# Kernel optimization log

Hardware: AMD Instinct MI355X
Metric: run time of the kernel (lower is better)

Reference implementation:

```python
import jax, jax.numpy as jnp
import numpy as np

EMBED_DIM = 1024
NUM_HEADS = 16
D_K = EMBED_DIM // NUM_HEADS
SEQ = 4096
BATCH = 1


def setup_inputs() -> dict:
    key = jax.random.key(0)
    ks = jax.random.split(key, 9)
    s = 1.0 / np.sqrt(EMBED_DIM)
    return {
        "x": jax.random.normal(ks[0], (BATCH, SEQ, EMBED_DIM), dtype=jnp.float32),
        "Wq": jax.random.normal(ks[1], (EMBED_DIM, EMBED_DIM), dtype=jnp.float32) * s,
        "bq": jax.random.normal(ks[2], (EMBED_DIM,), dtype=jnp.float32) * 0.02,
        "Wk": jax.random.normal(ks[3], (EMBED_DIM, EMBED_DIM), dtype=jnp.float32) * s,
        "bk": jax.random.normal(ks[4], (EMBED_DIM,), dtype=jnp.float32) * 0.02,
        "Wv": jax.random.normal(ks[5], (EMBED_DIM, EMBED_DIM), dtype=jnp.float32) * s,
        "bv": jax.random.normal(ks[6], (EMBED_DIM,), dtype=jnp.float32) * 0.02,
        "Wo": jax.random.normal(ks[7], (EMBED_DIM, EMBED_DIM), dtype=jnp.float32) * s,
        "bo": jax.random.normal(ks[8], (EMBED_DIM,), dtype=jnp.float32) * 0.02,
    }


def reference(x, Wq, bq, Wk, bk, Wv, bv, Wo, bo):
    B, S, E = x.shape
    H, Dk = NUM_HEADS, D_K

    def split_heads(t):  # [B,S,E] -> [B,H,S,Dk]
        return t.reshape(B, S, H, Dk).transpose(0, 2, 1, 3)

    Q = split_heads(x @ Wq.T + bq)
    K = split_heads(x @ Wk.T + bk)
    V = split_heads(x @ Wv.T + bv)

    scores = jnp.einsum("bhqd,bhkd->bhqk", Q, K) / jnp.sqrt(jnp.float32(Dk))
    causal = jnp.tril(jnp.ones((S, S), dtype=bool))
    scores = jnp.where(causal, scores, -jnp.inf)
    attn = jax.nn.softmax(scores, axis=-1)
    out = jnp.einsum("bhqk,bhkd->bhqd", attn, V)  # [B,H,S,Dk]
    out = out.transpose(0, 2, 1, 3).reshape(B, S, E)
    return out @ Wo.T + bo
```

## Files before the change

kernel.cpp:

```cpp
#include <hip/hip_runtime.h>
#include <hip/hip_bf16.h>
#include <math.h>

#define SEQ 4096
#define EMB 1024
#define NH  16
#define DK  64

typedef __attribute__((ext_vector_type(8))) unsigned short us8;
typedef __attribute__((ext_vector_type(8))) short         s8;
typedef __attribute__((ext_vector_type(4))) unsigned short us4;
typedef __attribute__((ext_vector_type(4))) float          f4;

static __device__ __forceinline__ unsigned short f2bf(float f) {
    union { float f; unsigned u; } v; v.f = f;
    unsigned r = v.u + 0x7FFF + ((v.u >> 16) & 1);
    return (unsigned short)(r >> 16);
}

__device__ __forceinline__ void gl2lds16(const void* g, void* l) {
    __builtin_amdgcn_global_load_lds((const __attribute__((address_space(1))) void*)g,
                                     (__attribute__((address_space(3))) void*)l, 16, 0, 0);
}

__device__ __forceinline__ int pkbf(float a, float b) {
    return (int)__builtin_amdgcn_perm(__float_as_uint(a), __float_as_uint(b), 0x07060302u);
}

__global__ void cvt_all(const float* __restrict__ x,
                        const float* __restrict__ w0, const float* __restrict__ w1,
                        const float* __restrict__ w2, const float* __restrict__ w3,
                        unsigned short* __restrict__ xo,
                        unsigned short* __restrict__ o0, unsigned short* __restrict__ o1,
                        unsigned short* __restrict__ o2, unsigned short* __restrict__ o3) {
    const int idx = blockIdx.x * 256 + threadIdx.x;
    const float* in;
    unsigned short* out;
    int off;
    if (idx < (1 << 20)) { in = x; out = xo; off = idx; }
    else {
        const int t = idx - (1 << 20);
        const int w = t >> 18;
        off = t & ((1 << 18) - 1);
        in  = w == 0 ? w0 : (w == 1 ? w1 : (w == 2 ? w2 : w3));
        out = w == 0 ? o0 : (w == 1 ? o1 : (w == 2 ? o2 : o3));
    }
    const float4 v = ((const float4*)in)[off];
    us4 o;
    o[0] = f2bf(v.x); o[1] = f2bf(v.y); o[2] = f2bf(v.z); o[3] = f2bf(v.w);
    ((us4*)out)[off] = o;
}

__global__ __launch_bounds__(256) void transpose_kernel(
    const unsigned short* __restrict__ in, unsigned short* __restrict__ out) {
    __shared__ unsigned short t[64][72];
    const int tid = threadIdx.x;
    const int row = tid >> 2, c = (tid & 3) * 16;
    const int gr = blockIdx.x * 64, gc = blockIdx.y * 64;
    const unsigned short* src = in + (size_t)(gr + row) * EMB + gc + c;
    *(us8*)&t[row][c]     = *(const us8*)src;
    *(us8*)&t[row][c + 8] = *(const us8*)(src + 8);
    __syncthreads();
    us8 o0, o1;
#pragma unroll
    for (int j = 0; j < 8; ++j) { o0[j] = t[c + j][row]; o1[j] = t[c + 8 + j][row]; }
    const int a_   = c >> 4;
    const int base = (a_ >> 1) * 32 + (a_ & 1) * 4;
    us4 g0, g1, g2, g3;
#pragma unroll
    for (int i = 0; i < 4; ++i) { g0[i] = o0[i]; g1[i] = o0[4 + i]; g2[i] = o1[i]; g3[i] = o1[4 + i]; }
    unsigned short* dst = out + (size_t)(gc + row) * SEQ + gr + base;
    *(us4*)dst        = g0;
    *(us4*)(dst + 8)  = g1;
    *(us4*)(dst + 16) = g2;
    *(us4*)(dst + 24) = g3;
}

__global__ __launch_bounds__(256) void qkv_gemm(
    const unsigned short* __restrict__ X,
    const unsigned short* __restrict__ Wq, const unsigned short* __restrict__ Wk,
    const unsigned short* __restrict__ Wv,
    const float* __restrict__ bq, const float* __restrict__ bk, const float* __restrict__ bv,
    unsigned short* __restrict__ Qo, unsigned short* __restrict__ Ko, unsigned short* __restrict__ Vo)
{
    __shared__ unsigned short As[128 * 64];
    __shared__ unsigned short Bs[128 * 64];

    const int region = blockIdx.y >> 3;
    const unsigned short* W   = region == 0 ? Wq : (region == 1 ? Wk : Wv);
    const float*         bias = region == 0 ? bq : (region == 1 ? bk : bv);
    unsigned short*      out  = region == 0 ? Qo : (region == 1 ? Ko : Vo);
    const float scale = region == 0 ? 0.18033688011112042f : 1.0f;

    const int tid  = threadIdx.x;
    const int wave = tid >> 6;
    const int lane = tid & 63;
    const int quad = lane >> 4;
    const int l16  = lane & 15;
    const int wm   = (wave >> 1) * 64;
    const int wn   = (wave & 1) * 64;
    const int bm   = blockIdx.x * 128;
    const int bn   = (blockIdx.y & 7) * 128;

    f4 acc[4][4];
#pragma unroll
    for (int a = 0; a < 4; ++a)
#pragma unroll
        for (int b = 0; b < 4; ++b) acc[a][b] = (f4){0, 0, 0, 0};

    const int rsub = lane >> 3;
    const int gc   = ((lane & 7) ^ rsub) * 8;
    const int swz  = l16 & 7;

    for (int k0 = 0; k0 < EMB; k0 += 64) {
        __syncthreads();
#pragma unroll
        for (int i = 0; i < 4; ++i) {
            const int cb = i * 4 + wave;
            const int r  = cb * 8 + rsub;
            gl2lds16(X + (size_t)(bm + r) * EMB + k0 + gc, &As[cb * 512]);
            gl2lds16(W + (size_t)(bn + r) * EMB + k0 + gc, &Bs[cb * 512]);
        }
        __syncthreads();
#pragma unroll
        for (int kc = 0; kc < 2; ++kc) {
            s8 af[4], bf[4];
#pragma unroll
            for (int t = 0; t < 4; ++t) {
                const int seg = (kc * 4 + quad) ^ swz;
                af[t] = *(const s8*)&As[(wm + t * 16 + l16) * 64 + seg * 8];
                bf[t] = *(const s8*)&Bs[(wn + t * 16 + l16) * 64 + seg * 8];
            }
#pragma unroll
            for (int tm = 0; tm < 4; ++tm)
#pragma unroll
                for (int tn = 0; tn < 4; ++tn)
                    acc[tm][tn] = __builtin_amdgcn_mfma_f32_16x16x32_bf16(af[tm], bf[tn], acc[tm][tn], 0, 0, 0);
        }
    }

#pragma unroll
    for (int tn = 0; tn < 4; ++tn) {
        const int n = bn + wn + tn * 16 + l16;
        const float bv2 = bias[n];
#pragma unroll
        for (int tm = 0; tm < 4; ++tm)
#pragma unroll
            for (int rr = 0; rr < 4; ++rr) {
                const int m = bm + wm + tm * 16 + quad * 4 + rr;
                out[(size_t)m * EMB + n] = f2bf((acc[tm][tn][rr] + bv2) * scale);
            }
    }
}

__global__ __launch_bounds__(256) void gemm_op(
    const unsigned short* __restrict__ A, const unsigned short* __restrict__ B,
    const float* __restrict__ bias, float* __restrict__ C)
{
    __shared__ unsigned short As[128 * 64];
    __shared__ unsigned short Bs[64 * 64];

    const int tid  = threadIdx.x;
    const int wave = tid >> 6;
    const int lane = tid & 63;
    const int quad = lane >> 4;
    const int l16  = lane & 15;
    const int wm   = (wave >> 1) * 64;
    const int wn   = (wave & 1) * 32;
    const int bm   = blockIdx.x * 128;
    const int bn   = blockIdx.y * 64;

    f4 acc[4][2];
#pragma unroll
    for (int a = 0; a < 4; ++a) { acc[a][0] = (f4){0,0,0,0}; acc[a][1] = (f4){0,0,0,0}; }

    const int rsub = lane >> 3;
    const int gc   = ((lane & 7) ^ rsub) * 8;
    const int swz  = l16 & 7;

    for (int k0 = 0; k0 < EMB; k0 += 64) {
        __syncthreads();
#pragma unroll
        for (int i = 0; i < 6; ++i) {
            const int cb = i * 4 + wave;
            if (cb < 16) {
                gl2lds16(A + (size_t)(bm + cb * 8 + rsub) * EMB + k0 + gc, &As[cb * 512]);
            } else {
                const int c2 = cb - 16;
                gl2lds16(B + (size_t)(bn + c2 * 8 + rsub) * EMB + k0 + gc, &Bs[c2 * 512]);
            }
        }
        __syncthreads();
#pragma unroll
        for (int kc = 0; kc < 2; ++kc) {
            const int seg = (kc * 4 + quad) ^ swz;
            s8 af[4], bf[2];
#pragma unroll
            for (int t = 0; t < 4; ++t)
                af[t] = *(const s8*)&As[(wm + t * 16 + l16) * 64 + seg * 8];
#pragma unroll
            for (int t = 0; t < 2; ++t)
                bf[t] = *(const s8*)&Bs[(wn + t * 16 + l16) * 64 + seg * 8];
#pragma unroll
            for (int tm = 0; tm < 4; ++tm)
#pragma unroll
                for (int tn = 0; tn < 2; ++tn)
                    acc[tm][tn] = __builtin_amdgcn_mfma_f32_16x16x32_bf16(af[tm], bf[tn], acc[tm][tn], 0, 0, 0);
        }
    }

#pragma unroll
    for (int tn = 0; tn < 2; ++tn) {
        const int n = bn + wn + tn * 16 + l16;
        const float bv2 = bias[n];
#pragma unroll
        for (int tm = 0; tm < 4; ++tm)
#pragma unroll
            for (int rr = 0; rr < 4; ++rr) {
                const int m = bm + wm + tm * 16 + quad * 4 + rr;
                C[(size_t)m * EMB + n] = acc[tm][tn][rr] + bv2;
            }
    }
}

__global__ __launch_bounds__(512) void attn_kernel(
    const unsigned short* __restrict__ Qg, const unsigned short* __restrict__ Kg,
    const unsigned short* __restrict__ Vtg, unsigned short* __restrict__ Og)
{
    __shared__ unsigned short Ks[2][128][72];
    __shared__ unsigned short Vs[2][128][72];

    const int tid  = threadIdx.x;
    const int wave = tid >> 6;
    const int lane = tid & 63;
    const int quad = lane >> 4;
    const int l16  = lane & 15;
    const int h    = blockIdx.x;
    const int y    = blockIdx.y;
    const int u    = (y < 16) ? y : 47 - y;
    const int jmax = 63 - u;
    const int jmine = (wave < 4) ? jmax : u;
    const int tileMine = (wave < 4) ? (63 - u) : u;
    const int colbase = h * DK;
    const int wrow0 = tileMine * 64 + (wave & 3) * 16;
    const int q_own = wrow0 + l16;

    s8 qf[2];
    {
        const unsigned short* q = Qg + (size_t)q_own * EMB + colbase + quad * 8;
        qf[0] = *(const s8*)(q);
        qf[1] = *(const s8*)(q + 32);
    }

    const int row = tid >> 3;
    const int c0  = (tid & 7) * 8;
    const unsigned short* kptr = Kg  + (size_t)row * EMB + colbase + c0;
    const unsigned short* vptr = Vtg + (size_t)(colbase + row) * SEQ + c0;

    const int imax = jmax >> 1;

    {
        us8 a = *(const us8*)kptr;
        us8 b = *(const us8*)(kptr + (size_t)64 * EMB);
        us8 c = *(const us8*)vptr;
        us8 d = *(const us8*)(vptr + 64);
        *(us8*)&Ks[0][row][c0]      = a;
        *(us8*)&Ks[0][64 + row][c0] = b;
        *(us8*)&Vs[0][row][c0]      = c;
        *(us8*)&Vs[0][64 + row][c0] = d;
    }
    us8 kre = *(const us8*)(kptr + (size_t)2 * 64 * EMB);
    us8 kro = *(const us8*)(kptr + (size_t)3 * 64 * EMB);
    us8 vre = *(const us8*)(vptr + 2 * 64);
    us8 vro = *(const us8*)(vptr + 3 * 64);

    float l_i = 0.0f;
    f4 o[4];
#pragma unroll
    for (int t = 0; t < 4; ++t) o[t] = (f4){0, 0, 0, 0};

    for (int i = 0; i <= imax; ++i) {
        __syncthreads();
        const int cur = i & 1;
        if (i < imax) {
            const int nxt = cur ^ 1;
            *(us8*)&Ks[nxt][row][c0]      = kre;
            *(us8*)&Ks[nxt][64 + row][c0] = kro;
            *(us8*)&Vs[nxt][row][c0]      = vre;
            *(us8*)&Vs[nxt][64 + row][c0] = vro;
            if (i + 1 < imax) {
                const int je = 2 * (i + 2);
                kre = *(const us8*)(kptr + (size_t)je * 64 * EMB);
                vre = *(const us8*)(vptr + je * 64);
                const int jo = je + 1;
                if (jo <= jmax) {
                    kro = *(const us8*)(kptr + (size_t)jo * 64 * EMB);
                    vro = *(const us8*)(vptr + jo * 64);
                }
            }
        }

#pragma unroll
        for (int sub = 0; sub < 2; ++sub) {
            const int j = 2 * i + sub;
            if (j <= jmine) {
                const int rb = sub * 64;
                f4 s[4] = { {0,0,0,0}, {0,0,0,0}, {0,0,0,0}, {0,0,0,0} };
#pragma unroll
                for (int kc = 0; kc < 2; ++kc)
#pragma unroll
                    for (int t = 0; t < 4; ++t) {
                        s8 kv = *(const s8*)&Ks[cur][rb + t * 16 + l16][kc * 32 + quad * 8];
                        s[t] = __builtin_amdgcn_mfma_f32_16x16x32_bf16(kv, qf[kc], s[t], 0, 0, 0);
                    }

                if (j == jmine) {
#pragma unroll
                    for (int t = 0; t < 4; ++t) {
                        const int kb = j * 64 + t * 16 + quad * 4;
#pragma unroll
                        for (int r = 0; r < 4; ++r)
                            if (kb + r > q_own) s[t][r] = -1e30f;
                    }
                }

                float rs = 0.0f;
#pragma unroll
                for (int t = 0; t < 4; ++t)
#pragma unroll
                    for (int r = 0; r < 4; ++r) {
                        const float p = __builtin_amdgcn_exp2f(s[t][r]);
                        s[t][r] = p;
                        rs += p;
                    }
                rs += __shfl_xor(rs, 16);
                rs += __shfl_xor(rs, 32);
                l_i += rs;

                union { int i[8]; s8 v[2]; } pku;
#pragma unroll
                for (int t = 0; t < 4; ++t) {
                    pku.i[t * 2]     = pkbf(s[t][1], s[t][0]);
                    pku.i[t * 2 + 1] = pkbf(s[t][3], s[t][2]);
                }

#pragma unroll
                for (int kc = 0; kc < 2; ++kc)
#pragma unroll
                    for (int t = 0; t < 4; ++t) {
                        s8 va = *(const s8*)&Vs[cur][rb + t * 16 + l16][kc * 32 + quad * 8];
                        o[t] = __builtin_amdgcn_mfma_f32_16x16x32_bf16(va, pku.v[kc], o[t], 0, 0, 0);
                    }
            }
        }
    }

    const float inv = 1.0f / l_i;
#pragma unroll
    for (int t = 0; t < 4; ++t) {
        us4 ov;
#pragma unroll
        for (int r = 0; r < 4; ++r) ov[r] = f2bf(o[t][r] * inv);
        *(us4*)&Og[(size_t)q_own * EMB + colbase + t * 16 + quad * 4] = ov;
    }
}

extern "C" void kernel_launch(void* const* d_in, const int* in_sizes, int n_in,
                              void* d_out, int out_size, void* d_ws, size_t ws_size,
                              hipStream_t stream) {
    const float* x  = (const float*)d_in[0];
    const float* Wq = (const float*)d_in[1];
    const float* bq = (const float*)d_in[2];
    const float* Wk = (const float*)d_in[3];
    const float* bk = (const float*)d_in[4];
    const float* Wv = (const float*)d_in[5];
    const float* bv = (const float*)d_in[6];
    const float* Wo = (const float*)d_in[7];
    const float* bo = (const float*)d_in[8];
    float* out = (float*)d_out;

    unsigned short* ws = (unsigned short*)d_ws;
    unsigned short* xb  = ws;
    unsigned short* Wqb = xb  + (size_t)SEQ * EMB;
    unsigned short* Wkb = Wqb + (size_t)EMB * EMB;
    unsigned short* Wvb = Wkb + (size_t)EMB * EMB;
    unsigned short* Wob = Wvb + (size_t)EMB * EMB;
    unsigned short* Qb  = Wob + (size_t)EMB * EMB;
    unsigned short* Kb  = Qb  + (size_t)SEQ * EMB;
    unsigned short* Vtb = Kb  + (size_t)SEQ * EMB;
    unsigned short* Ab  = Vtb + (size_t)SEQ * EMB;

    cvt_all<<<8192, 256, 0, stream>>>(x, Wq, Wk, Wv, Wo, xb, Wqb, Wkb, Wvb, Wob);

    qkv_gemm<<<dim3(SEQ / 128, 24), 256, 0, stream>>>(xb, Wqb, Wkb, Wvb, bq, bk, bv, Qb, Kb, Ab);

    transpose_kernel<<<dim3(SEQ / 64, EMB / 64), 256, 0, stream>>>(Ab, Vtb);

    attn_kernel<<<dim3(NH, 32), 512, 0, stream>>>(Qb, Kb, Vtb, Ab);

    gemm_op<<<dim3(SEQ / 128, EMB / 64), 256, 0, stream>>>(Ab, Wob, bo, out);
}
```

Before: 206.1 us.

## Split attention key tiles across wave pairs with swizzled async LDS loads

Restructures the attention kernel so each wave handles 32 query rows and only one parity of the two key sub-tiles per step, instead of 16 rows over both sub-tiles. The per-parity partial outputs and row sums are then merged through LDS at the end. K/V staging moves from register-staged copies to direct global-to-LDS loads into an XOR-swizzled layout without padding, and MFMA sections get raised wave priority plus a launch-bounds occupancy hint. The aim is more reuse of each K/V fragment across query rows, fewer register round trips and fewer LDS bank conflicts. The cost is an extra LDS reduction pass with two more barriers and higher register pressure.

```diff
diff --git a/kernel.cpp b/kernel.cpp
--- a/kernel.cpp
+++ b/kernel.cpp
@@ -223,12 +223,12 @@
     }
 }
 
-__global__ __launch_bounds__(512) void attn_kernel(
+__global__ __launch_bounds__(512, 4) void attn_kernel(
     const unsigned short* __restrict__ Qg, const unsigned short* __restrict__ Kg,
     const unsigned short* __restrict__ Vtg, unsigned short* __restrict__ Og)
 {
-    __shared__ unsigned short Ks[2][128][72];
-    __shared__ unsigned short Vs[2][128][72];
+    __shared__ unsigned short Ks[2][2][64][64];
+    __shared__ unsigned short Vs[2][2][64][64];
 
     const int tid  = threadIdx.x;
     const int wave = tid >> 6;
@@ -239,129 +239,169 @@
     const int y    = blockIdx.y;
     const int u    = (y < 16) ? y : 47 - y;
     const int jmax = 63 - u;
-    const int jmine = (wave < 4) ? jmax : u;
     const int tileMine = (wave < 4) ? (63 - u) : u;
+    const int par  = (wave >> 1) & 1;
+    const int qh   = wave & 1;
+    const int jmine = tileMine;
     const int colbase = h * DK;
-    const int wrow0 = tileMine * 64 + (wave & 3) * 16;
-    const int q_own = wrow0 + l16;
-
-    s8 qf[2];
+    const int wrow0 = tileMine * 64 + qh * 32;
+    const int q0    = wrow0 + l16;
+
+    s8 qf00, qf10, qf01, qf11;
     {
-        const unsigned short* q = Qg + (size_t)q_own * EMB + colbase + quad * 8;
-        qf[0] = *(const s8*)(q);
-        qf[1] = *(const s8*)(q + 32);
-    }
-
-    const int row = tid >> 3;
-    const int c0  = (tid & 7) * 8;
-    const unsigned short* kptr = Kg  + (size_t)row * EMB + colbase + c0;
-    const unsigned short* vptr = Vtg + (size_t)(colbase + row) * SEQ + c0;
+        const unsigned short* q = Qg + (size_t)q0 * EMB + colbase + quad * 8;
+        qf00 = *(const s8*)(q);
+        qf10 = *(const s8*)(q + 32);
+        qf01 = *(const s8*)(q + (size_t)16 * EMB);
+        qf11 = *(const s8*)(q + (size_t)16 * EMB + 32);
+    }
+
+    const int xr    = (l16 & 7) << 4;
+    const int coff0 = ((quad * 16) ^ xr) >> 1;
+    const int coff1 = (((64) + quad * 16) ^ xr) >> 1;
+
+    const int srow = tid >> 3;
+    const int scol = (((tid & 7) * 16) ^ ((srow & 7) << 4)) >> 1;
+    const unsigned short* ksrc = Kg  + (size_t)srow * EMB + colbase + scol;
+    const unsigned short* vsrc = Vtg + (size_t)(colbase + srow) * SEQ + scol;
 
     const int imax = jmax >> 1;
 
-    {
-        us8 a = *(const us8*)kptr;
-        us8 b = *(const us8*)(kptr + (size_t)64 * EMB);
-        us8 c = *(const us8*)vptr;
-        us8 d = *(const us8*)(vptr + 64);
-        *(us8*)&Ks[0][row][c0]      = a;
-        *(us8*)&Ks[0][64 + row][c0] = b;
-        *(us8*)&Vs[0][row][c0]      = c;
-        *(us8*)&Vs[0][64 + row][c0] = d;
-    }
-    us8 kre = *(const us8*)(kptr + (size_t)2 * 64 * EMB);
-    us8 kro = *(const us8*)(kptr + (size_t)3 * 64 * EMB);
-    us8 vre = *(const us8*)(vptr + 2 * 64);
-    us8 vro = *(const us8*)(vptr + 3 * 64);
-
-    float l_i = 0.0f;
-    f4 o[4];
-#pragma unroll
-    for (int t = 0; t < 4; ++t) o[t] = (f4){0, 0, 0, 0};
+    gl2lds16(ksrc,                    &Ks[0][0][wave * 8][0]);
+    gl2lds16(vsrc,                    &Vs[0][0][wave * 8][0]);
+    gl2lds16(ksrc + (size_t)64 * EMB, &Ks[0][1][wave * 8][0]);
+    gl2lds16(vsrc + 64,               &Vs[0][1][wave * 8][0]);
+
+    float l0 = 0.0f, l1 = 0.0f;
+    f4 o0[4], o1[4];
+#pragma unroll
+    for (int t = 0; t < 4; ++t) { o0[t] = (f4){0, 0, 0, 0}; o1[t] = (f4){0, 0, 0, 0}; }
 
     for (int i = 0; i <= imax; ++i) {
         __syncthreads();
         const int cur = i & 1;
         if (i < imax) {
             const int nxt = cur ^ 1;
-            *(us8*)&Ks[nxt][row][c0]      = kre;
-            *(us8*)&Ks[nxt][64 + row][c0] = kro;
-            *(us8*)&Vs[nxt][row][c0]      = vre;
-            *(us8*)&Vs[nxt][64 + row][c0] = vro;
-            if (i + 1 < imax) {
-                const int je = 2 * (i + 2);
-                kre = *(const us8*)(kptr + (size_t)je * 64 * EMB);
-                vre = *(const us8*)(vptr + je * 64);
-                const int jo = je + 1;
-                if (jo <= jmax) {
-                    kro = *(const us8*)(kptr + (size_t)jo * 64 * EMB);
-                    vro = *(const us8*)(vptr + jo * 64);
-                }
-            }
-        }
-
-#pragma unroll
-        for (int sub = 0; sub < 2; ++sub) {
-            const int j = 2 * i + sub;
-            if (j <= jmine) {
-                const int rb = sub * 64;
-                f4 s[4] = { {0,0,0,0}, {0,0,0,0}, {0,0,0,0}, {0,0,0,0} };
-#pragma unroll
-                for (int kc = 0; kc < 2; ++kc)
-#pragma unroll
-                    for (int t = 0; t < 4; ++t) {
-                        s8 kv = *(const s8*)&Ks[cur][rb + t * 16 + l16][kc * 32 + quad * 8];
-                        s[t] = __builtin_amdgcn_mfma_f32_16x16x32_bf16(kv, qf[kc], s[t], 0, 0, 0);
-                    }
-
-                if (j == jmine) {
-#pragma unroll
-                    for (int t = 0; t < 4; ++t) {
-                        const int kb = j * 64 + t * 16 + quad * 4;
-#pragma unroll
-                        for (int r = 0; r < 4; ++r)
-                            if (kb + r > q_own) s[t][r] = -1e30f;
+            const int je  = 2 * (i + 1);
+            gl2lds16(ksrc + (size_t)je * 64 * EMB, &Ks[nxt][0][wave * 8][0]);
+            gl2lds16(vsrc + (size_t)je * 64,       &Vs[nxt][0][wave * 8][0]);
+            const int jo = je + 1;
+            if (jo <= jmax) {
+                gl2lds16(ksrc + (size_t)jo * 64 * EMB, &Ks[nxt][1][wave * 8][0]);
+                gl2lds16(vsrc + (size_t)jo * 64,       &Vs[nxt][1][wave * 8][0]);
+            }
+        }
+
+        const int j = 2 * i + par;
+        if (j <= jmine) {
+            const unsigned short* KsP = &Ks[cur][par][0][0];
+            const unsigned short* VsP = &Vs[cur][par][0][0];
+
+            f4 s0[4] = { {0,0,0,0}, {0,0,0,0}, {0,0,0,0}, {0,0,0,0} };
+            f4 s1[4] = { {0,0,0,0}, {0,0,0,0}, {0,0,0,0}, {0,0,0,0} };
+            __builtin_amdgcn_s_setprio(1);
+#pragma unroll
+            for (int t = 0; t < 4; ++t) {
+                const int rbase = (t * 16 + l16) * 64;
+                s8 kv0 = *(const s8*)&KsP[rbase + coff0];
+                s8 kv1 = *(const s8*)&KsP[rbase + coff1];
+                s0[t] = __builtin_amdgcn_mfma_f32_16x16x32_bf16(kv0, qf00, s0[t], 0, 0, 0);
+                s1[t] = __builtin_amdgcn_mfma_f32_16x16x32_bf16(kv0, qf01, s1[t], 0, 0, 0);
+                s0[t] = __builtin_amdgcn_mfma_f32_16x16x32_bf16(kv1, qf10, s0[t], 0, 0, 0);
+                s1[t] = __builtin_amdgcn_mfma_f32_16x16x32_bf16(kv1, qf11, s1[t], 0, 0, 0);
+            }
+            __builtin_amdgcn_s_setprio(0);
+
+            if (j == jmine) {
+#pragma unroll
+                for (int t = 0; t < 4; ++t) {
+                    const int kb = j * 64 + t * 16 + quad * 4;
+#pragma unroll
+                    for (int r = 0; r < 4; ++r) {
+                        if (kb + r > q0)      s0[t][r] = -1e30f;
+                        if (kb + r > q0 + 16) s1[t][r] = -1e30f;
                     }
                 }
-
-                float rs = 0.0f;
-#pragma unroll
-                for (int t = 0; t < 4; ++t)
-#pragma unroll
-                    for (int r = 0; r < 4; ++r) {
-                        const float p = __builtin_amdgcn_exp2f(s[t][r]);
-                        s[t][r] = p;
-                        rs += p;
-                    }
-                rs += __shfl_xor(rs, 16);
-                rs += __shfl_xor(rs, 32);
-                l_i += rs;
-
-                union { int i[8]; s8 v[2]; } pku;
-#pragma unroll
-                for (int t = 0; t < 4; ++t) {
-                    pku.i[t * 2]     = pkbf(s[t][1], s[t][0]);
-                    pku.i[t * 2 + 1] = pkbf(s[t][3], s[t][2]);
+            }
+
+            float rs0 = 0.0f, rs1 = 0.0f;
+#pragma unroll
+            for (int t = 0; t < 4; ++t)
+#pragma unroll
+                for (int r = 0; r < 4; ++r) {
+                    const float p0 = __builtin_amdgcn_exp2f(s0[t][r]);
+                    const float p1 = __builtin_amdgcn_exp2f(s1[t][r]);
+                    s0[t][r] = p0; rs0 += p0;
+                    s1[t][r] = p1; rs1 += p1;
                 }
-
-#pragma unroll
-                for (int kc = 0; kc < 2; ++kc)
-#pragma unroll
-                    for (int t = 0; t < 4; ++t) {
-                        s8 va = *(const s8*)&Vs[cur][rb + t * 16 + l16][kc * 32 + quad * 8];
-                        o[t] = __builtin_amdgcn_mfma_f32_16x16x32_bf16(va, pku.v[kc], o[t], 0, 0, 0);
-                    }
-            }
-        }
-    }
-
-    const float inv = 1.0f / l_i;
-#pragma unroll
-    for (int t = 0; t < 4; ++t) {
-        us4 ov;
-#pragma unroll
-        for (int r = 0; r < 4; ++r) ov[r] = f2bf(o[t][r] * inv);
-        *(us4*)&Og[(size_t)q_own * EMB + colbase + t * 16 + quad * 4] = ov;
+            rs0 += __shfl_xor(rs0, 16);
+            rs0 += __shfl_xor(rs0, 32);
+            rs1 += __shfl_xor(rs1, 16);
+            rs1 += __shfl_xor(rs1, 32);
+            l0 += rs0;
+            l1 += rs1;
+
+            union { int i[8]; s8 v[2]; } pk0, pk1;
+#pragma unroll
+            for (int t = 0; t < 4; ++t) {
+                pk0.i[t * 2]     = pkbf(s0[t][1], s0[t][0]);
+                pk0.i[t * 2 + 1] = pkbf(s0[t][3], s0[t][2]);
+                pk1.i[t * 2]     = pkbf(s1[t][1], s1[t][0]);
+                pk1.i[t * 2 + 1] = pkbf(s1[t][3], s1[t][2]);
+            }
+
+            __builtin_amdgcn_s_setprio(1);
+#pragma unroll
+            for (int t = 0; t < 4; ++t) {
+                const int rbase = (t * 16 + l16) * 64;
+                s8 va0 = *(const s8*)&VsP[rbase + coff0];
+                s8 va1 = *(const s8*)&VsP[rbase + coff1];
+                o0[t] = __builtin_amdgcn_mfma_f32_16x16x32_bf16(va0, pk0.v[0], o0[t], 0, 0, 0);
+                o1[t] = __builtin_amdgcn_mfma_f32_16x16x32_bf16(va0, pk1.v[0], o1[t], 0, 0, 0);
+                o0[t] = __builtin_amdgcn_mfma_f32_16x16x32_bf16(va1, pk0.v[1], o0[t], 0, 0, 0);
+                o1[t] = __builtin_amdgcn_mfma_f32_16x16x32_bf16(va1, pk1.v[1], o1[t], 0, 0, 0);
+            }
+            __builtin_amdgcn_s_setprio(0);
+        }
+    }
+
+    __syncthreads();
+    float* mO = (float*)&Ks[0][0][0][0];
+    float* mL = (float*)&Vs[0][0][0][0];
+    const int slot = (wave >> 2) * 2 + qh;
+    const int mrow = slot * 64 + lane;
+    char* mp = (char*)mO + (size_t)mrow * 128;
+    const int msw = (lane & 7) << 4;
+    if (par == 1) {
+#pragma unroll
+        for (int t = 0; t < 4; ++t) {
+            *(f4*)(mp + ((t * 32)      ^ msw)) = o0[t];
+            *(f4*)(mp + ((t * 32 + 16) ^ msw)) = o1[t];
+        }
+        mL[mrow * 2]     = l0;
+        mL[mrow * 2 + 1] = l1;
+    }
+    __syncthreads();
+    if (par == 0) {
+#pragma unroll
+        for (int t = 0; t < 4; ++t) {
+            o0[t] += *(const f4*)(mp + ((t * 32)      ^ msw));
+            o1[t] += *(const f4*)(mp + ((t * 32 + 16) ^ msw));
+        }
+        l0 += mL[mrow * 2];
+        l1 += mL[mrow * 2 + 1];
+        const float inv0 = 1.0f / l0;
+        const float inv1 = 1.0f / l1;
+#pragma unroll
+        for (int t = 0; t < 4; ++t) {
+            us4 ov;
+#pragma unroll
+            for (int r = 0; r < 4; ++r) ov[r] = f2bf(o0[t][r] * inv0);
+            *(us4*)&Og[(size_t)q0 * EMB + colbase + t * 16 + quad * 4] = ov;
+#pragma unroll
+            for (int r = 0; r < 4; ++r) ov[r] = f2bf(o1[t][r] * inv1);
+            *(us4*)&Og[(size_t)(q0 + 16) * EMB + colbase + t * 16 + quad * 4] = ov;
+        }
     }
 }
 
```

Result: faster. 199.0 us (-3.4%).
